# Optimization experiments

Hardware: AMD Instinct MI355X
Metric: run time of the kernel (lower is better)

Reference implementation:

```python
import jax, jax.numpy as jnp
import numpy as np

B, S, D, H = 2, 2048, 1024, 16
DH = D // H
EPS = 1e-5


def _ln(x, g, b):
    m = jnp.mean(x, axis=-1, keepdims=True)
    v = jnp.mean((x - m) ** 2, axis=-1, keepdims=True)
    return (x - m) * jax.lax.rsqrt(v + EPS) * g + b


def setup_inputs() -> dict:
    key = jax.random.key(0)
    ks = jax.random.split(key, 16)
    w = lambda k, shp: jax.random.normal(k, shp, jnp.float32) * 0.02
    return {
        "x": jax.random.normal(ks[0], (B, S, D), jnp.float32),
        # semantic preprocessor: Linear(D,2D) -> ReLU -> Linear(2D,D), residual + LN
        "pW1": w(ks[1], (D, 2 * D)), "pb1": jnp.zeros((2 * D,), jnp.float32),
        "pW2": w(ks[2], (2 * D, D)), "pb2": jnp.zeros((D,), jnp.float32),
        "gp": jnp.ones((D,), jnp.float32), "bp": jnp.zeros((D,), jnp.float32),
        # multi-head attention projections
        "Wq": w(ks[3], (D, D)), "bq": jnp.zeros((D,), jnp.float32),
        "Wk": w(ks[4], (D, D)), "bk": jnp.zeros((D,), jnp.float32),
        "Wv": w(ks[5], (D, D)), "bv": jnp.zeros((D,), jnp.float32),
        "Wo": w(ks[6], (D, D)), "bo": jnp.zeros((D,), jnp.float32),
        "g1": jnp.ones((D,), jnp.float32), "b1": jnp.zeros((D,), jnp.float32),
        # FFN: Linear(D,4D) -> ReLU -> Linear(4D,D)
        "Wf1": w(ks[7], (D, 4 * D)), "bf1": jnp.zeros((4 * D,), jnp.float32),
        "Wf2": w(ks[8], (4 * D, D)), "bf2": jnp.zeros((D,), jnp.float32),
        "g2": jnp.ones((D,), jnp.float32), "b2": jnp.zeros((D,), jnp.float32),
    }


def reference(x, pW1, pb1, pW2, pb2, gp, bp,
              Wq, bq, Wk, bk, Wv, bv, Wo, bo, g1, b1,
              Wf1, bf1, Wf2, bf2, g2, b2):
    # specialized 'semantic' preprocessor (dropout = identity in eval)
    h = jax.nn.relu(x @ pW1 + pb1) @ pW2 + pb2
    s = _ln(x + h, gp, bp)                       # [B,S,D]
    # naive multi-head attention
    q = (s @ Wq + bq).reshape(B, S, H, DH)
    k = (s @ Wk + bk).reshape(B, S, H, DH)
    v = (s @ Wv + bv).reshape(B, S, H, DH)
    scores = jnp.einsum("bqhd,bkhd->bhqk", q, k) / np.sqrt(DH).astype(np.float32)
    attn = jax.nn.softmax(scores, axis=-1)       # [B,H,S,S]
    ctx = jnp.einsum("bhqk,bkhd->bqhd", attn, v).reshape(B, S, D)
    attn_out = ctx @ Wo + bo
    y = _ln(s + attn_out, g1, b1)
    # FFN (dropouts = identity)
    f = jax.nn.relu(y @ Wf1 + bf1) @ Wf2 + bf2
    return _ln(y + f, g2, b2)
```

## Files before the change

### kernel.cpp

```cpp
#include <hip/hip_runtime.h>
#include <cstdint>
#include <cstddef>

typedef _Float16 f16;
typedef _Float16 f16x8 __attribute__((ext_vector_type(8)));
typedef _Float16 f16x4 __attribute__((ext_vector_type(4)));
typedef float    f32x4 __attribute__((ext_vector_type(4)));
typedef float    f32x16 __attribute__((ext_vector_type(16)));
typedef unsigned int uint2v __attribute__((ext_vector_type(2)));

#define MFMA16(a,b,c) __builtin_amdgcn_mfma_f32_16x16x32_f16(a, b, c, 0, 0, 0)
#define MFMA32(a,b,c) __builtin_amdgcn_mfma_f32_32x32x16_f16(a, b, c, 0, 0, 0)

static __device__ __forceinline__ void gload_lds16(const void* g, void* l) {
  __builtin_amdgcn_global_load_lds(
      (const __attribute__((address_space(1))) unsigned int*)g,
      (__attribute__((address_space(3))) unsigned int*)l, 16, 0, 0);
}

static __device__ __forceinline__ int pkh(float a, float b) {
  auto t = __builtin_amdgcn_cvt_pkrtz(a, b);
  return __builtin_bit_cast(int, t);
}

static __device__ __forceinline__ float ex2(float x) {
  return __builtin_amdgcn_exp2f(x);
}

static __device__ __forceinline__ uint2v pswap(int a, int b) {
  return __builtin_amdgcn_permlane32_swap((unsigned)a, (unsigned)b, false, false);
}
static __device__ __forceinline__ float xhalf_max(float x) {
  uint2v r = pswap(__builtin_bit_cast(int, x), __builtin_bit_cast(int, x));
  return fmaxf(__builtin_bit_cast(float, r.x), __builtin_bit_cast(float, r.y));
}
static __device__ __forceinline__ float f3(float a, float b, float c) {
  return fmaxf(fmaxf(a, b), c);
}

static __device__ __forceinline__ void wtrans_blk(float (*tile)[33],
                                                  const float* __restrict__ W,
                                                  f16* __restrict__ Wt,
                                                  int K, int N, int gx,
                                                  float scale, int lb) {
  const int n0 = (lb % gx) * 32, k0 = (lb / gx) * 32;
  const int c = threadIdx.x & 31, r = threadIdx.x >> 5;
#pragma unroll
  for (int i = 0; i < 4; i++) {
    int row = r + i * 8;
    tile[row][c] = W[(size_t)(k0 + row) * N + n0 + c];
  }
  __syncthreads();
#pragma unroll
  for (int i = 0; i < 4; i++) {
    int row = r + i * 8;
    Wt[(size_t)(n0 + row) * K + k0 + c] = (f16)(tile[c][row] * scale);
  }
}

__global__ __launch_bounds__(256)
void prep_kernel(const float* __restrict__ x, f16* __restrict__ xb,
                 const float* __restrict__ pW1, f16* __restrict__ wtP1,
                 const float* __restrict__ pW2, f16* __restrict__ wtP2,
                 const float* __restrict__ Wq,  f16* __restrict__ wtQ,
                 const float* __restrict__ Wk,  f16* __restrict__ wtK,
                 const float* __restrict__ Wv,  f16* __restrict__ wtV,
                 const float* __restrict__ Wo,  f16* __restrict__ wtO,
                 const float* __restrict__ Wf1, f16* __restrict__ wtF1,
                 const float* __restrict__ Wf2, f16* __restrict__ wtF2,
                 const float* __restrict__ bq, const float* __restrict__ bk,
                 const float* __restrict__ bv, float* __restrict__ bqkv) {
  __shared__ float tile[32][33];
  int b = blockIdx.x;
  if (b < 4096) {
    int i = b * 256 + threadIdx.x;
    float4 v = ((const float4*)x)[i];
    f16x4 h;
    h[0] = (f16)v.x; h[1] = (f16)v.y; h[2] = (f16)v.z; h[3] = (f16)v.w;
    *(f16x4*)(xb + (size_t)i * 4) = h;
    return;
  }
  b -= 4096;
  if (b < 2048) { wtrans_blk(tile, pW1, wtP1, 1024, 2048, 64, 1.f, b); return; }
  b -= 2048;
  if (b < 2048) { wtrans_blk(tile, pW2, wtP2, 2048, 1024, 32, 1.f, b); return; }
  b -= 2048;
  if (b < 1024) { wtrans_blk(tile, Wq, wtQ, 1024, 1024, 32, 0.18033688f, b); return; }
  b -= 1024;
  if (b < 1024) { wtrans_blk(tile, Wk, wtK, 1024, 1024, 32, 1.f, b); return; }
  b -= 1024;
  if (b < 1024) { wtrans_blk(tile, Wv, wtV, 1024, 1024, 32, 1.f, b); return; }
  b -= 1024;
  if (b < 1024) { wtrans_blk(tile, Wo, wtO, 1024, 1024, 32, 1.f, b); return; }
  b -= 1024;
  if (b < 4096) { wtrans_blk(tile, Wf1, wtF1, 1024, 4096, 128, 1.f, b); return; }
  b -= 4096;
  if (b < 4096) { wtrans_blk(tile, Wf2, wtF2, 4096, 1024, 32, 1.f, b); return; }
  b -= 4096;
  {
    int i = b * 256 + threadIdx.x;
    if (i < 1024)       bqkv[i] = bq[i] * 0.18033688f;
    else if (i < 2048)  bqkv[i] = bk[i - 1024];
    else if (i < 3072)  bqkv[i] = bv[i - 2048];
  }
}

template <int MODE, bool PF>
__global__ __launch_bounds__(256, 2)
void gemm_kernel(const f16* __restrict__ A, const f16* __restrict__ W,
                 const float* __restrict__ bias, void* __restrict__ out,
                 f16* __restrict__ vt, int N, int K, int gx) {
  constexpr int BUFS = PF ? 2 : 1;
  __shared__ __align__(16) f16 lsA[BUFS * 128 * 64];
  __shared__ __align__(16) f16 lsB[BUFS * 128 * 64];
  const int tid  = threadIdx.x;
  const int lane = tid & 63;
  const int wid  = tid >> 6;
  const int frow = lane & 15;
  const int kgrp = lane >> 4;
  const int wmBase = (wid >> 1) * 64;
  const int wnBase = (wid & 1) * 64;

  const int bid = blockIdx.x;
  const int xcd = bid & 7, slot = bid >> 3;
  const int bm = (xcd << 2) + slot / gx;
  const int bn = slot % gx;

  const f32x4 zero4 = {0.f, 0.f, 0.f, 0.f};
  f32x4 acc[4][4];
#pragma unroll
  for (int i = 0; i < 4; i++)
#pragma unroll
    for (int j = 0; j < 4; j++) acc[i][j] = zero4;

  const f16* aSrc[4]; int lOffA[4];
  const f16* bSrc[4];
#pragma unroll
  for (int i = 0; i < 4; i++) {
    int c_lin = i * 256 + wid * 64 + lane;
    int row = c_lin >> 3;
    int ch  = (c_lin & 7) ^ (row & 7);
    aSrc[i] = A + (size_t)(bm * 128 + row) * K + ch * 8;
    bSrc[i] = W + (size_t)(bn * 128 + row) * K + ch * 8;
    lOffA[i] = (i * 256 + wid * 64) * 8;
  }

  auto compute = [&](const f16* la, const f16* lb) {
#pragma unroll
    for (int kk = 0; kk < 2; kk++) {
      f16x8 af[4], bf[4];
#pragma unroll
      for (int i = 0; i < 4; i++) {
        int row = wmBase + i * 16 + frow;
        af[i] = *(const f16x8*)&la[row * 64 + (((kk * 4 + kgrp) ^ (row & 7)) << 3)];
      }
#pragma unroll
      for (int j = 0; j < 4; j++) {
        int row = wnBase + j * 16 + frow;
        bf[j] = *(const f16x8*)&lb[row * 64 + (((kk * 4 + kgrp) ^ (row & 7)) << 3)];
      }
#pragma unroll
      for (int i = 0; i < 4; i++)
#pragma unroll
        for (int j = 0; j < 4; j++) acc[i][j] = MFMA16(af[i], bf[j], acc[i][j]);
    }
  };

  const int nk = K >> 6;
  if constexpr (PF) {
#define GST(T, PB)                                                        \
    {                                                                     \
      f16* la = lsA + (PB) * 8192;                                        \
      f16* lb = lsB + (PB) * 8192;                                        \
      _Pragma("unroll") for (int i = 0; i < 4; i++) {                     \
        gload_lds16(aSrc[i] + (size_t)(T) * 64, la + lOffA[i]);           \
        gload_lds16(bSrc[i] + (size_t)(T) * 64, lb + lOffA[i]);           \
      }                                                                   \
    }
    GST(0, 0);
    for (int ks = 0; ks < nk; ++ks) {
      const int nt = (ks + 1 < nk) ? ks + 1 : nk - 1;
      GST(nt, (ks + 1) & 1);
      asm volatile("s_waitcnt vmcnt(8)" ::: "memory");
      __builtin_amdgcn_s_barrier();
      compute(lsA + (ks & 1) * 8192, lsB + (ks & 1) * 8192);
      __builtin_amdgcn_s_barrier();
    }
    asm volatile("s_waitcnt vmcnt(0)" ::: "memory");
#undef GST
  } else {
    for (int ks = 0; ks < nk; ++ks) {
#pragma unroll
      for (int i = 0; i < 4; i++) {
        gload_lds16(aSrc[i] + (size_t)ks * 64, &lsA[lOffA[i]]);
        gload_lds16(bSrc[i] + (size_t)ks * 64, &lsB[lOffA[i]]);
      }
      __syncthreads();
      compute(lsA, lsB);
      __syncthreads();
    }
  }

#pragma unroll
  for (int j = 0; j < 4; j++) {
    const int col = bn * 128 + wnBase + j * 16 + frow;
    const float bb = bias[col];
#pragma unroll
    for (int i = 0; i < 4; i++) {
      const int row0 = bm * 128 + wmBase + i * 16 + kgrp * 4;
      if (MODE == 3 && col >= 2048) {
        const int vcol = col - 2048;
        const int bh = (row0 >> 11) * 16 + (vcol >> 6);
        const int d  = vcol & 63;
        const int kv = row0 & 2047;
        f16x4 pk;
#pragma unroll
        for (int r = 0; r < 4; r++) pk[r] = (f16)(acc[i][j][r] + bb);
        *(f16x4*)(vt + ((size_t)bh * 64 + d) * 2048 + kv) = pk;
      } else {
#pragma unroll
        for (int r = 0; r < 4; r++) {
          float v = acc[i][j][r] + bb;
          if (MODE == 1) v = fmaxf(v, 0.f);
          ((f16*)out)[(size_t)(row0 + r) * N + col] = (f16)v;
        }
      }
    }
  }
}

__global__ __launch_bounds__(256, 2)
void gemm_splitk(const f16* __restrict__ A, const f16* __restrict__ W,
                 f16* __restrict__ outp, int K) {
  __shared__ __align__(16) f16 lsA[2 * 128 * 64];
  __shared__ __align__(16) f16 lsB[2 * 128 * 64];
  const int tid  = threadIdx.x;
  const int lane = tid & 63;
  const int wid  = tid >> 6;
  const int frow = lane & 15;
  const int kgrp = lane >> 4;
  const int wmBase = (wid >> 1) * 64;
  const int wnBase = (wid & 1) * 64;

  const int bid = blockIdx.x;
  const int xcd = bid & 7, slot = bid >> 3;
  const int q = slot >> 3, bn = slot & 7;
  const int bmkp = xcd * 8 + q;
  const int bm = bmkp >> 1, kp = bmkp & 1;
  const int Kh = K >> 1;
  const f16* Ab = A + kp * Kh;
  const f16* Wb = W + kp * Kh;

  const f32x4 zero4 = {0.f, 0.f, 0.f, 0.f};
  f32x4 acc[4][4];
#pragma unroll
  for (int i = 0; i < 4; i++)
#pragma unroll
    for (int j = 0; j < 4; j++) acc[i][j] = zero4;

  const f16* aSrc[4]; const f16* bSrc[4]; int lOff[4];
#pragma unroll
  for (int i = 0; i < 4; i++) {
    int c_lin = i * 256 + wid * 64 + lane;
    int row = c_lin >> 3;
    int ch  = (c_lin & 7) ^ (row & 7);
    aSrc[i] = Ab + (size_t)(bm * 128 + row) * K + ch * 8;
    bSrc[i] = Wb + (size_t)(bn * 128 + row) * K + ch * 8;
    lOff[i] = (i * 256 + wid * 64) * 8;
  }

  auto compute = [&](const f16* la, const f16* lb) {
#pragma unroll
    for (int kk = 0; kk < 2; kk++) {
      f16x8 af[4], bf[4];
#pragma unroll
      for (int i = 0; i < 4; i++) {
        int row = wmBase + i * 16 + frow;
        af[i] = *(const f16x8*)&la[row * 64 + (((kk * 4 + kgrp) ^ (row & 7)) << 3)];
      }
#pragma unroll
      for (int j = 0; j < 4; j++) {
        int row = wnBase + j * 16 + frow;
        bf[j] = *(const f16x8*)&lb[row * 64 + (((kk * 4 + kgrp) ^ (row & 7)) << 3)];
      }
#pragma unroll
      for (int i = 0; i < 4; i++)
#pragma unroll
        for (int j = 0; j < 4; j++) acc[i][j] = MFMA16(af[i], bf[j], acc[i][j]);
    }
  };

#define GST(T, PB)                                                        \
  {                                                                       \
    f16* la = lsA + (PB) * 8192;                                          \
    f16* lb = lsB + (PB) * 8192;                                          \
    _Pragma("unroll") for (int i = 0; i < 4; i++) {                       \
      gload_lds16(aSrc[i] + (size_t)(T) * 64, la + lOff[i]);              \
      gload_lds16(bSrc[i] + (size_t)(T) * 64, lb + lOff[i]);              \
    }                                                                     \
  }
  const int nk = Kh >> 6;
  GST(0, 0);
  for (int ks = 0; ks < nk; ++ks) {
    const int nt = (ks + 1 < nk) ? ks + 1 : nk - 1;
    GST(nt, (ks + 1) & 1);
    asm volatile("s_waitcnt vmcnt(8)" ::: "memory");
    __builtin_amdgcn_s_barrier();
    compute(lsA + (ks & 1) * 8192, lsB + (ks & 1) * 8192);
    __builtin_amdgcn_s_barrier();
  }
  asm volatile("s_waitcnt vmcnt(0)" ::: "memory");
#undef GST

  f16* op = outp + (size_t)kp * 4096 * 1024;
#pragma unroll
  for (int j = 0; j < 4; j++) {
    const int col = bn * 128 + wnBase + j * 16 + frow;
#pragma unroll
    for (int i = 0; i < 4; i++) {
      const int row0 = bm * 128 + wmBase + i * 16 + kgrp * 4;
#pragma unroll
      for (int r = 0; r < 4; r++)
        op[(size_t)(row0 + r) * 1024 + col] = (f16)acc[i][j][r];
    }
  }
}

__global__ __launch_bounds__(256)
void ln_res2(const f16* __restrict__ p, const f16* __restrict__ res,
             const float* __restrict__ bias, const float* __restrict__ g,
             const float* __restrict__ be, float* __restrict__ of,
             f16* __restrict__ ob) {
  const int row = blockIdx.x, t = threadIdx.x;
  const size_t off = (size_t)row * 1024 + t * 4;
  const f16x4 a = *(const f16x4*)(p + off);
  const f16x4 b = *(const f16x4*)(p + (size_t)4096 * 1024 + off);
  const f16x4 rr = *(const f16x4*)(res + off);
  const float4 bb = ((const float4*)bias)[t];
  float v0 = (float)a[0] + (float)b[0] + bb.x + (float)rr[0];
  float v1 = (float)a[1] + (float)b[1] + bb.y + (float)rr[1];
  float v2 = (float)a[2] + (float)b[2] + bb.z + (float)rr[2];
  float v3 = (float)a[3] + (float)b[3] + bb.w + (float)rr[3];
  float s = v0 + v1 + v2 + v3;
  float q = v0 * v0 + v1 * v1 + v2 * v2 + v3 * v3;
#pragma unroll
  for (int o = 1; o < 64; o <<= 1) {
    s += __shfl_xor(s, o);
    q += __shfl_xor(q, o);
  }
  __shared__ float ss[4], sq[4];
  if ((t & 63) == 0) { ss[t >> 6] = s; sq[t >> 6] = q; }
  __syncthreads();
  s = ss[0] + ss[1] + ss[2] + ss[3];
  q = sq[0] + sq[1] + sq[2] + sq[3];
  const float mean = s * (1.f / 1024.f);
  const float var  = q * (1.f / 1024.f) - mean * mean;
  const float rstd = rsqrtf(var + 1e-5f);
  const float4 gv = ((const float4*)g)[t];
  const float4 bv = ((const float4*)be)[t];
  float4 ov;
  ov.x = (v0 - mean) * rstd * gv.x + bv.x;
  ov.y = (v1 - mean) * rstd * gv.y + bv.y;
  ov.z = (v2 - mean) * rstd * gv.z + bv.z;
  ov.w = (v3 - mean) * rstd * gv.w + bv.w;
  if (of) ((float4*)(of + (size_t)row * 1024))[t] = ov;
  if (ob) {
    f16x4 hv;
    hv[0] = (f16)ov.x; hv[1] = (f16)ov.y; hv[2] = (f16)ov.z; hv[3] = (f16)ov.w;
    *(f16x4*)(ob + off) = hv;
  }
}

__global__ __launch_bounds__(256, 4)
void attn_kernel(const f16* __restrict__ Qp, const f16* __restrict__ Kp,
                 const f16* __restrict__ Vt, f16* __restrict__ opart,
                 float* __restrict__ Lbuf, int ldq) {
  __shared__ __align__(16) f16 lsKb[2 * 64 * 64];
  __shared__ __align__(16) f16 lsVb[2 * 64 * 64];
  const int tid = threadIdx.x, lane = tid & 63, wid = tid >> 6;
  const int qcol = lane & 31;
  const int hi = lane >> 5;
  const int bid = blockIdx.x;
  const int idx = bid >> 3;
  const int bh = ((bid & 7) << 2) | (idx & 3);
  const int rest = idx >> 2;
  const int part = rest & 1;
  const int qt = rest >> 1;
  const int b = bh >> 4, h = bh & 15;
  const size_t rb = (size_t)b * 2048;
  const int hc = h * 64;
  const int kv0 = part * 1024;
  const int qrow = qt * 128 + wid * 32 + qcol;

  f16x8 qf[4];
  {
    const f16* qp = Qp + (rb + qrow) * ldq + hc;
#pragma unroll
    for (int kc = 0; kc < 4; kc++) qf[kc] = *(const f16x8*)(qp + kc * 16 + hi * 8);
  }
  f16x8 ones;
#pragma unroll
  for (int i = 0; i < 8; i++) ones[i] = (f16)1.0f;

  f32x16 ot0, ot1, lacc;
#pragma unroll
  for (int i = 0; i < 16; i++) { ot0[i] = 0.f; ot1[i] = 0.f; lacc[i] = 0.f; }
  float mrun = -1e30f;

  const f16 *kS0, *kS1, *vS0, *vS1;
  int off0, off1;
  {
    int c0 = wid * 64 + lane;
    int r0 = c0 >> 3, ch0 = (c0 & 7) ^ (r0 & 7);
    int c1 = 256 + wid * 64 + lane;
    int r1 = c1 >> 3, ch1 = (c1 & 7) ^ (r1 & 7);
    kS0 = Kp + (rb + kv0 + r0) * ldq + hc + ch0 * 8;
    kS1 = Kp + (rb + kv0 + r1) * ldq + hc + ch1 * 8;
    const f16* vbase = Vt + (size_t)bh * 64 * 2048 + kv0;
    vS0 = vbase + (size_t)r0 * 2048 + ch0 * 8;
    vS1 = vbase + (size_t)r1 * 2048 + ch1 * 8;
    off0 = (wid * 64) * 8;
    off1 = (256 + wid * 64) * 8;
  }

#define ASTAGE(T, PB)                                                    \
  {                                                                      \
    f16* kd = lsKb + (PB) * 4096;                                        \
    f16* vd = lsVb + (PB) * 4096;                                        \
    const size_t ko = (size_t)(T) * 64 * ldq;                            \
    const size_t vo = (size_t)(T) * 64;                                  \
    gload_lds16(kS0 + ko, kd + off0);                                    \
    gload_lds16(kS1 + ko, kd + off1);                                    \
    gload_lds16(vS0 + vo, vd + off0);                                    \
    gload_lds16(vS1 + vo, vd + off1);                                    \
  }

  ASTAGE(0, 0);
  asm volatile("s_waitcnt vmcnt(0)" ::: "memory");
  __builtin_amdgcn_s_barrier();

  for (int kt = 0; kt < 16; ++kt) {
    const int cur = kt & 1;
    if (kt < 15) ASTAGE(kt + 1, cur ^ 1);
    const f16* kb = lsKb + cur * 4096;
    const f16* vb = lsVb + cur * 4096;

    f32x16 s0, s1;
#pragma unroll
    for (int i = 0; i < 16; i++) { s0[i] = 0.f; s1[i] = 0.f; }
    const int kr0 = qcol, kr1 = 32 + qcol;
    __builtin_amdgcn_s_setprio(1);
#pragma unroll
    for (int kc = 0; kc < 4; kc++) {
      f16x8 a0 = *(const f16x8*)&kb[kr0 * 64 + (((kc * 2 + hi) ^ (kr0 & 7)) << 3)];
      f16x8 a1 = *(const f16x8*)&kb[kr1 * 64 + (((kc * 2 + hi) ^ (kr1 & 7)) << 3)];
      s0 = MFMA32(a0, qf[kc], s0);
      s1 = MFMA32(a1, qf[kc], s1);
    }
    __builtin_amdgcn_s_setprio(0);

    float t10[11];
#pragma unroll
    for (int r = 0; r < 10; r++) {
      float e0 = (3 * r + 0 < 16) ? s0[(3 * r + 0) & 15] : s1[(3 * r + 0) & 15];
      float e1 = (3 * r + 1 < 16) ? s0[(3 * r + 1) & 15] : s1[(3 * r + 1) & 15];
      float e2 = (3 * r + 2 < 16) ? s0[(3 * r + 2) & 15] : s1[(3 * r + 2) & 15];
      t10[r] = f3(e0, e1, e2);
    }
    t10[10] = fmaxf(s1[14], s1[15]);
    float p0 = f3(t10[0], t10[1], t10[2]);
    float p1 = f3(t10[3], t10[4], t10[5]);
    float p2 = f3(t10[6], t10[7], t10[8]);
    float p3 = fmaxf(t10[9], t10[10]);
    float pmax = xhalf_max(fmaxf(fmaxf(p0, p1), fmaxf(p2, p3)));
    if (__any(pmax > mrun + 11.54f)) {
      float mn = fmaxf(mrun, pmax);
      float fac = ex2(mrun - mn);
      mrun = mn;
#pragma unroll
      for (int i = 0; i < 16; i++) {
        ot0[i] *= fac; ot1[i] *= fac; lacc[i] *= fac;
      }
    }
#pragma unroll
    for (int r = 0; r < 16; r++) {
      s0[r] = ex2(s0[r] - mrun);
      s1[r] = ex2(s1[r] - mrun);
    }

#pragma unroll
    for (int st = 0; st < 2; ++st) {
#pragma unroll
      for (int c0 = 0; c0 < 2; c0++) {
        const int c8 = c0 * 8;
        int a0, a1, b0, b1;
        if (st == 0) {
          a0 = pkh(s0[c8 + 0], s0[c8 + 1]); a1 = pkh(s0[c8 + 2], s0[c8 + 3]);
          b0 = pkh(s0[c8 + 4], s0[c8 + 5]); b1 = pkh(s0[c8 + 6], s0[c8 + 7]);
        } else {
          a0 = pkh(s1[c8 + 0], s1[c8 + 1]); a1 = pkh(s1[c8 + 2], s1[c8 + 3]);
          b0 = pkh(s1[c8 + 4], s1[c8 + 5]); b1 = pkh(s1[c8 + 6], s1[c8 + 7]);
        }
        uint2v r0 = pswap(a0, b0);
        uint2v r1 = pswap(a1, b1);
        int4 wv;
        wv.x = (int)r0.x; wv.y = (int)r1.x; wv.z = (int)r0.y; wv.w = (int)r1.y;
        f16x8 pfrag = __builtin_bit_cast(f16x8, wv);
        const int ch = st * 4 + c0 * 2 + hi;
        const int vr0 = qcol, vr1 = 32 + qcol;
        f16x8 av0 = *(const f16x8*)&vb[vr0 * 64 + ((ch ^ (vr0 & 7)) << 3)];
        f16x8 av1 = *(const f16x8*)&vb[vr1 * 64 + ((ch ^ (vr1 & 7)) << 3)];
        __builtin_amdgcn_s_setprio(1);
        ot0 = MFMA32(av0, pfrag, ot0);
        ot1 = MFMA32(av1, pfrag, ot1);
        lacc = MFMA32(ones, pfrag, lacc);
        __builtin_amdgcn_s_setprio(0);
      }
    }
    asm volatile("s_waitcnt vmcnt(0)" ::: "memory");
    __builtin_amdgcn_s_barrier();
  }
#undef ASTAGE

  const float lfin = lacc[0];
  const float rinv = 1.f / lfin;
  const size_t pbase = ((size_t)part * 32 + bh) * 2048 + qrow;
  f16* pp = opart + pbase * 64;
#pragma unroll
  for (int rr = 0; rr < 16; rr += 2) {
    const int d = (rr & 3) + 8 * (rr >> 2) + 4 * hi;
    *(int*)(pp + d)      = pkh(ot0[rr] * rinv, ot0[rr + 1] * rinv);
    *(int*)(pp + 32 + d) = pkh(ot1[rr] * rinv, ot1[rr + 1] * rinv);
  }
  if (hi == 0) Lbuf[pbase] = mrun + __builtin_amdgcn_logf(lfin);
}

__global__ __launch_bounds__(256)
void combine_kernel(const f16* __restrict__ opart, const float* __restrict__ Lbuf,
                    f16* __restrict__ ctx) {
  const int bid = blockIdx.x;
  const int bh = bid >> 5, qblk = bid & 31;
  const int t = threadIdx.x;
  const int q = qblk * 64 + (t >> 2);
  const int dp = (t & 3) * 16;
  const size_t base = (size_t)bh * 2048 + q;
  const size_t p1o = (size_t)32 * 2048;
  const float L0 = Lbuf[base];
  const float L1 = Lbuf[p1o + base];
  const float L = fmaxf(L0, L1);
  float w0 = ex2(L0 - L), w1 = ex2(L1 - L);
  const float rs = 1.f / (w0 + w1);
  w0 *= rs; w1 *= rs;
  const f16* p0 = opart + base * 64 + dp;
  const f16* p1 = opart + (p1o + base) * 64 + dp;
  f16x8 a0 = *(const f16x8*)p0, a1 = *(const f16x8*)(p0 + 8);
  f16x8 c0 = *(const f16x8*)p1, c1 = *(const f16x8*)(p1 + 8);
  f16x8 o0, o1;
#pragma unroll
  for (int j = 0; j < 8; j++) {
    o0[j] = (f16)(w0 * (float)a0[j] + w1 * (float)c0[j]);
    o1[j] = (f16)(w0 * (float)a1[j] + w1 * (float)c1[j]);
  }
  const int b = bh >> 4, h = bh & 15;
  f16* op = ctx + ((size_t)b * 2048 + q) * 1024 + h * 64 + dp;
  *(f16x8*)op = o0;
  *(f16x8*)(op + 8) = o1;
}

extern "C" void kernel_launch(void* const* d_in, const int* in_sizes, int n_in,
                              void* d_out, int out_size, void* d_ws, size_t ws_size,
                              hipStream_t stream) {
  const float* x   = (const float*)d_in[0];
  const float* pW1 = (const float*)d_in[1];
  const float* pb1 = (const float*)d_in[2];
  const float* pW2 = (const float*)d_in[3];
  const float* pb2 = (const float*)d_in[4];
  const float* gp  = (const float*)d_in[5];
  const float* bp  = (const float*)d_in[6];
  const float* Wq  = (const float*)d_in[7];
  const float* bq  = (const float*)d_in[8];
  const float* Wk  = (const float*)d_in[9];
  const float* bk  = (const float*)d_in[10];
  const float* Wv  = (const float*)d_in[11];
  const float* bv  = (const float*)d_in[12];
  const float* Wo  = (const float*)d_in[13];
  const float* bo  = (const float*)d_in[14];
  const float* g1  = (const float*)d_in[15];
  const float* b1  = (const float*)d_in[16];
  const float* Wf1 = (const float*)d_in[17];
  const float* bf1 = (const float*)d_in[18];
  const float* Wf2 = (const float*)d_in[19];
  const float* bf2 = (const float*)d_in[20];
  const float* g2  = (const float*)d_in[21];
  const float* b2  = (const float*)d_in[22];

  char* ws = (char*)d_ws;
  const size_t MB = 1024 * 1024;
  if (ws_size < 121 * MB) return;

  f16*   wtP1 = (f16*)(ws);
  f16*   wtP2 = (f16*)(ws + 4 * MB);
  f16*   wtQ  = (f16*)(ws + 8 * MB);
  f16*   wtO  = (f16*)(ws + 14 * MB);
  f16*   wtF1 = (f16*)(ws + 16 * MB);
  f16*   wtF2 = (f16*)(ws + 24 * MB);
  f16*   big  = (f16*)(ws + 32 * MB);
  f16*   xb   = (f16*)(ws + 64 * MB);
  f16*   sb   = (f16*)(ws + 72 * MB);
  f16*   ybuf = (f16*)(ws + 80 * MB);
  f16*   ctx  = (f16*)(ws + 88 * MB);
  f16*   part = (f16*)(ws + 96 * MB);
  f16*   opart= (f16*)(ws + 96 * MB);
  float* Lbuf = (float*)(ws + 112 * MB);
  float* bqkv = (float*)(ws + 112 * MB + 512 * 1024);
  f16*   wtK  = wtQ + (size_t)1024 * 1024;
  f16*   wtV  = wtQ + (size_t)2048 * 1024;
  f16*   Vt   = big + (size_t)4096 * 3072;

  dim3 blk(256);
  prep_kernel<<<20492, blk, 0, stream>>>(x, xb, pW1, wtP1, pW2, wtP2,
                                         Wq, wtQ, Wk, wtK, Wv, wtV, Wo, wtO,
                                         Wf1, wtF1, Wf2, wtF2, bq, bk, bv, bqkv);

  gemm_kernel<1, true><<<512, blk, 0, stream>>>(xb, wtP1, pb1, big, nullptr, 2048, 1024, 16);
  gemm_splitk<<<512, blk, 0, stream>>>(big, wtP2, part, 2048);
  ln_res2<<<4096, blk, 0, stream>>>(part, xb, pb2, gp, bp, nullptr, sb);
  gemm_kernel<3, false><<<768, blk, 0, stream>>>(sb, wtQ, bqkv, big, Vt, 3072, 1024, 24);
  attn_kernel<<<1024, blk, 0, stream>>>(big, big + 1024, Vt, opart, Lbuf, 3072);
  combine_kernel<<<1024, blk, 0, stream>>>(opart, Lbuf, ctx);
  gemm_splitk<<<512, blk, 0, stream>>>(ctx, wtO, part, 1024);
  ln_res2<<<4096, blk, 0, stream>>>(part, sb, bo, g1, b1, nullptr, ybuf);
  gemm_kernel<1, false><<<1024, blk, 0, stream>>>(ybuf, wtF1, bf1, big, nullptr, 4096, 1024, 32);
  gemm_splitk<<<512, blk, 0, stream>>>(big, wtF2, part, 4096);
  ln_res2<<<4096, blk, 0, stream>>>(part, ybuf, bf2, g2, b2, (float*)d_out, nullptr);
}
```

Baseline: 271.5 us.

## Fuse attention combine into split-K output GEMM and widen split-K to four

Removes the standalone combine kernel by merging the two attention partials (weighted by their log-sum-exp values) directly into LDS inside the Wo split-K GEMM. It also templates split-K on the partition count, uses four partitions for the P2 and F2 GEMMs with twice the blocks, and raises launch_bounds occupancy to 4. The GEMM main loop drops double-buffered async prefetch for a single buffer with __syncthreads, trading latency hiding for occupancy. Four-way split-K doubles the partial-sum traffic that the LayerNorm kernels must read.

```diff
diff --git a/kernel.cpp b/kernel.cpp
--- a/kernel.cpp
+++ b/kernel.cpp
@@ -229,11 +229,12 @@
   }
 }
 
-__global__ __launch_bounds__(256, 2)
+template <int KP, bool COMBINE>
+__global__ __launch_bounds__(256, 4)
 void gemm_splitk(const f16* __restrict__ A, const f16* __restrict__ W,
-                 f16* __restrict__ outp, int K) {
-  __shared__ __align__(16) f16 lsA[2 * 128 * 64];
-  __shared__ __align__(16) f16 lsB[2 * 128 * 64];
+                 f16* __restrict__ outp, int K, const float* __restrict__ Lb) {
+  __shared__ __align__(16) f16 lsA[128 * 64];
+  __shared__ __align__(16) f16 lsB[128 * 64];
   const int tid  = threadIdx.x;
   const int lane = tid & 63;
   const int wid  = tid >> 6;
@@ -244,10 +245,10 @@
 
   const int bid = blockIdx.x;
   const int xcd = bid & 7, slot = bid >> 3;
-  const int q = slot >> 3, bn = slot & 7;
-  const int bmkp = xcd * 8 + q;
-  const int bm = bmkp >> 1, kp = bmkp & 1;
-  const int Kh = K >> 1;
+  const int qq = slot >> 3, bn = slot & 7;
+  const int bmkp = xcd * (KP * 4) + qq;
+  const int bm = bmkp / KP, kp = bmkp % KP;
+  const int Kh = K / KP;
   const f16* Ab = A + kp * Kh;
   const f16* Wb = W + kp * Kh;
 
@@ -259,58 +260,65 @@
     for (int j = 0; j < 4; j++) acc[i][j] = zero4;
 
   const f16* aSrc[4]; const f16* bSrc[4]; int lOff[4];
+  int rowA[4], chA[4];
 #pragma unroll
   for (int i = 0; i < 4; i++) {
     int c_lin = i * 256 + wid * 64 + lane;
     int row = c_lin >> 3;
     int ch  = (c_lin & 7) ^ (row & 7);
+    rowA[i] = bm * 128 + row;
+    chA[i] = ch;
     aSrc[i] = Ab + (size_t)(bm * 128 + row) * K + ch * 8;
     bSrc[i] = Wb + (size_t)(bn * 128 + row) * K + ch * 8;
     lOff[i] = (i * 256 + wid * 64) * 8;
   }
 
-  auto compute = [&](const f16* la, const f16* lb) {
+  const int nk = Kh >> 6;
+  for (int ks = 0; ks < nk; ++ks) {
+#pragma unroll
+    for (int i = 0; i < 4; i++) gload_lds16(bSrc[i] + (size_t)ks * 64, &lsB[lOff[i]]);
+    if constexpr (COMBINE) {
+      const int h = kp * 8 + ks;
+#pragma unroll
+      for (int i = 0; i < 4; i++) {
+        const int q = rowA[i] & 2047, bb = rowA[i] >> 11;
+        const size_t lidx = (size_t)(bb * 16 + h) * 2048 + q;
+        const f16x8 p0 = *(const f16x8*)(A + lidx * 64 + chA[i] * 8);
+        const f16x8 p1 = *(const f16x8*)(A + (size_t)65536 * 64 + lidx * 64 + chA[i] * 8);
+        const float L0 = Lb[lidx];
+        const float L1 = Lb[65536 + lidx];
+        const float Lm = fmaxf(L0, L1);
+        const float w0 = ex2(L0 - Lm), w1 = ex2(L1 - Lm);
+        const float rs = 1.f / (w0 + w1);
+        const f16 W0 = (f16)(w0 * rs), W1 = (f16)(w1 * rs);
+        f16x8 cv = p0 * W0 + p1 * W1;
+        *(f16x8*)(lsA + lOff[i] + lane * 8) = cv;
+      }
+    } else {
+#pragma unroll
+      for (int i = 0; i < 4; i++) gload_lds16(aSrc[i] + (size_t)ks * 64, &lsA[lOff[i]]);
+    }
+    __syncthreads();
 #pragma unroll
     for (int kk = 0; kk < 2; kk++) {
       f16x8 af[4], bf[4];
 #pragma unroll
       for (int i = 0; i < 4; i++) {
         int row = wmBase + i * 16 + frow;
-        af[i] = *(const f16x8*)&la[row * 64 + (((kk * 4 + kgrp) ^ (row & 7)) << 3)];
+        af[i] = *(const f16x8*)&lsA[row * 64 + (((kk * 4 + kgrp) ^ (row & 7)) << 3)];
       }
 #pragma unroll
       for (int j = 0; j < 4; j++) {
         int row = wnBase + j * 16 + frow;
-        bf[j] = *(const f16x8*)&lb[row * 64 + (((kk * 4 + kgrp) ^ (row & 7)) << 3)];
+        bf[j] = *(const f16x8*)&lsB[row * 64 + (((kk * 4 + kgrp) ^ (row & 7)) << 3)];
       }
 #pragma unroll
       for (int i = 0; i < 4; i++)
 #pragma unroll
         for (int j = 0; j < 4; j++) acc[i][j] = MFMA16(af[i], bf[j], acc[i][j]);
     }
-  };
-
-#define GST(T, PB)                                                        \
-  {                                                                       \
-    f16* la = lsA + (PB) * 8192;                                          \
-    f16* lb = lsB + (PB) * 8192;                                          \
-    _Pragma("unroll") for (int i = 0; i < 4; i++) {                       \
-      gload_lds16(aSrc[i] + (size_t)(T) * 64, la + lOff[i]);              \
-      gload_lds16(bSrc[i] + (size_t)(T) * 64, lb + lOff[i]);              \
-    }                                                                     \
-  }
-  const int nk = Kh >> 6;
-  GST(0, 0);
-  for (int ks = 0; ks < nk; ++ks) {
-    const int nt = (ks + 1 < nk) ? ks + 1 : nk - 1;
-    GST(nt, (ks + 1) & 1);
-    asm volatile("s_waitcnt vmcnt(8)" ::: "memory");
-    __builtin_amdgcn_s_barrier();
-    compute(lsA + (ks & 1) * 8192, lsB + (ks & 1) * 8192);
-    __builtin_amdgcn_s_barrier();
-  }
-  asm volatile("s_waitcnt vmcnt(0)" ::: "memory");
-#undef GST
+    __syncthreads();
+  }
 
   f16* op = outp + (size_t)kp * 4096 * 1024;
 #pragma unroll
@@ -326,6 +334,7 @@
   }
 }
 
+template <int NP>
 __global__ __launch_bounds__(256)
 void ln_res2(const f16* __restrict__ p, const f16* __restrict__ res,
              const float* __restrict__ bias, const float* __restrict__ g,
@@ -333,14 +342,22 @@
              f16* __restrict__ ob) {
   const int row = blockIdx.x, t = threadIdx.x;
   const size_t off = (size_t)row * 1024 + t * 4;
-  const f16x4 a = *(const f16x4*)(p + off);
-  const f16x4 b = *(const f16x4*)(p + (size_t)4096 * 1024 + off);
+  float v0, v1, v2, v3;
+  {
+    const f16x4 a = *(const f16x4*)(p + off);
+    v0 = (float)a[0]; v1 = (float)a[1]; v2 = (float)a[2]; v3 = (float)a[3];
+  }
+#pragma unroll
+  for (int k = 1; k < NP; k++) {
+    const f16x4 a = *(const f16x4*)(p + (size_t)k * 4096 * 1024 + off);
+    v0 += (float)a[0]; v1 += (float)a[1]; v2 += (float)a[2]; v3 += (float)a[3];
+  }
   const f16x4 rr = *(const f16x4*)(res + off);
   const float4 bb = ((const float4*)bias)[t];
-  float v0 = (float)a[0] + (float)b[0] + bb.x + (float)rr[0];
-  float v1 = (float)a[1] + (float)b[1] + bb.y + (float)rr[1];
-  float v2 = (float)a[2] + (float)b[2] + bb.z + (float)rr[2];
-  float v3 = (float)a[3] + (float)b[3] + bb.w + (float)rr[3];
+  v0 += bb.x + (float)rr[0];
+  v1 += bb.y + (float)rr[1];
+  v2 += bb.z + (float)rr[2];
+  v3 += bb.w + (float)rr[3];
   float s = v0 + v1 + v2 + v3;
   float q = v0 * v0 + v1 * v1 + v2 * v2 + v3 * v3;
 #pragma unroll
@@ -533,38 +550,6 @@
     *(int*)(pp + 32 + d) = pkh(ot1[rr] * rinv, ot1[rr + 1] * rinv);
   }
   if (hi == 0) Lbuf[pbase] = mrun + __builtin_amdgcn_logf(lfin);
-}
-
-__global__ __launch_bounds__(256)
-void combine_kernel(const f16* __restrict__ opart, const float* __restrict__ Lbuf,
-                    f16* __restrict__ ctx) {
-  const int bid = blockIdx.x;
-  const int bh = bid >> 5, qblk = bid & 31;
-  const int t = threadIdx.x;
-  const int q = qblk * 64 + (t >> 2);
-  const int dp = (t & 3) * 16;
-  const size_t base = (size_t)bh * 2048 + q;
-  const size_t p1o = (size_t)32 * 2048;
-  const float L0 = Lbuf[base];
-  const float L1 = Lbuf[p1o + base];
-  const float L = fmaxf(L0, L1);
-  float w0 = ex2(L0 - L), w1 = ex2(L1 - L);
-  const float rs = 1.f / (w0 + w1);
-  w0 *= rs; w1 *= rs;
-  const f16* p0 = opart + base * 64 + dp;
-  const f16* p1 = opart + (p1o + base) * 64 + dp;
-  f16x8 a0 = *(const f16x8*)p0, a1 = *(const f16x8*)(p0 + 8);
-  f16x8 c0 = *(const f16x8*)p1, c1 = *(const f16x8*)(p1 + 8);
-  f16x8 o0, o1;
-#pragma unroll
-  for (int j = 0; j < 8; j++) {
-    o0[j] = (f16)(w0 * (float)a0[j] + w1 * (float)c0[j]);
-    o1[j] = (f16)(w0 * (float)a1[j] + w1 * (float)c1[j]);
-  }
-  const int b = bh >> 4, h = bh & 15;
-  f16* op = ctx + ((size_t)b * 2048 + q) * 1024 + h * 64 + dp;
-  *(f16x8*)op = o0;
-  *(f16x8*)(op + 8) = o1;
 }
 
 extern "C" void kernel_launch(void* const* d_in, const int* in_sizes, int n_in,
@@ -608,11 +593,11 @@
   f16*   xb   = (f16*)(ws + 64 * MB);
   f16*   sb   = (f16*)(ws + 72 * MB);
   f16*   ybuf = (f16*)(ws + 80 * MB);
-  f16*   ctx  = (f16*)(ws + 88 * MB);
-  f16*   part = (f16*)(ws + 96 * MB);
-  f16*   opart= (f16*)(ws + 96 * MB);
-  float* Lbuf = (float*)(ws + 112 * MB);
-  float* bqkv = (float*)(ws + 112 * MB + 512 * 1024);
+  f16*   part = (f16*)(ws + 88 * MB);
+  f16*   opart= (f16*)(ws + 88 * MB);
+  f16*   partO= (f16*)(ws + 104 * MB);
+  float* Lbuf = (float*)(ws + 120 * MB);
+  float* bqkv = (float*)(ws + 120 * MB + 512 * 1024);
   f16*   wtK  = wtQ + (size_t)1024 * 1024;
   f16*   wtV  = wtQ + (size_t)2048 * 1024;
   f16*   Vt   = big + (size_t)4096 * 3072;
@@ -623,14 +608,13 @@
                                          Wf1, wtF1, Wf2, wtF2, bq, bk, bv, bqkv);
 
   gemm_kernel<1, true><<<512, blk, 0, stream>>>(xb, wtP1, pb1, big, nullptr, 2048, 1024, 16);
-  gemm_splitk<<<512, blk, 0, stream>>>(big, wtP2, part, 2048);
-  ln_res2<<<4096, blk, 0, stream>>>(part, xb, pb2, gp, bp, nullptr, sb);
+  gemm_splitk<4, false><<<1024, blk, 0, stream>>>(big, wtP2, part, 2048, nullptr);
+  ln_res2<4><<<4096, blk, 0, stream>>>(part, xb, pb2, gp, bp, nullptr, sb);
   gemm_kernel<3, false><<<768, blk, 0, stream>>>(sb, wtQ, bqkv, big, Vt, 3072, 1024, 24);
   attn_kernel<<<1024, blk, 0, stream>>>(big, big + 1024, Vt, opart, Lbuf, 3072);
-  combine_kernel<<<1024, blk, 0, stream>>>(opart, Lbuf, ctx);
-  gemm_splitk<<<512, blk, 0, stream>>>(ctx, wtO, part, 1024);
-  ln_res2<<<4096, blk, 0, stream>>>(part, sb, bo, g1, b1, nullptr, ybuf);
+  gemm_splitk<2, true><<<512, blk, 0, stream>>>(opart, wtO, partO, 1024, Lbuf);
+  ln_res2<2><<<4096, blk, 0, stream>>>(partO, sb, bo, g1, b1, nullptr, ybuf);
   gemm_kernel<1, false><<<1024, blk, 0, stream>>>(ybuf, wtF1, bf1, big, nullptr, 4096, 1024, 32);
-  gemm_splitk<<<512, blk, 0, stream>>>(big, wtF2, part, 4096);
-  ln_res2<<<4096, blk, 0, stream>>>(part, ybuf, bf2, g2, b2, (float*)d_out, nullptr);
-}
+  gemm_splitk<4, false><<<1024, blk, 0, stream>>>(big, wtF2, part, 4096, nullptr);
+  ln_res2<4><<<4096, blk, 0, stream>>>(part, ybuf, bf2, g2, b2, (float*)d_out, nullptr);
+}
```

New measurement: 305.7 us. 12.6% more time.
